# Performance work log

Hardware: AMD Instinct MI355X
Metric: run time of the kernel (lower is better)

## Reference

```python
import jax, jax.numpy as jnp
import numpy as np
from jax import lax

TEMPERATURE = 30.0
PAD = 1  # padding init-kwarg; stride=1, dilation=1


def setup_inputs() -> dict:
    key = jax.random.key(0)
    ks = jax.random.split(key, 8)
    B, D, HID, NF, K, CIN, COUT, HW = 32, 512, 256, 8, 3, 64, 64, 64
    return {
        "filter_condition_input": jax.random.normal(ks[0], (B, D), jnp.float32),
        "model_input": jax.random.normal(ks[1], (B, CIN, HW, HW), jnp.float32),
        "fc1_w": jax.random.normal(ks[2], (HID, D), jnp.float32) * (2.0 / D) ** 0.5,
        "fc1_b": jnp.zeros((HID,), jnp.float32),
        "fc2_w": jax.random.normal(ks[3], (NF, HID), jnp.float32) * (2.0 / HID) ** 0.5,
        "fc2_b": jnp.zeros((NF,), jnp.float32),
        "weight": jax.random.normal(ks[4], (NF, COUT, CIN, K, K), jnp.float32) * 0.05,
        "bias_p": jax.random.normal(ks[5], (NF, COUT), jnp.float32) * 0.05,
    }


def reference(filter_condition_input, model_input, fc1_w, fc1_b, fc2_w, fc2_b, weight, bias_p):
    # Routing MLP -> softmax attention over the num_filters kernel bank
    h = jax.nn.relu(filter_condition_input @ fc1_w.T + fc1_b)
    logits = h @ fc2_w.T + fc2_b
    attn = jax.nn.softmax(logits / TEMPERATURE, axis=1)  # [B, NF]

    # Per-sample aggregated conv kernels and biases
    agg_w = jnp.einsum("bf,foikl->boikl", attn, weight)  # [B, O, Cin, K, K]
    agg_b = attn @ bias_p                                  # [B, O]

    # groups = batch_size grouped conv == independent per-sample conv (vmapped)
    def conv1(x_i, w_i):  # x_i: [Cin,H,W], w_i: [O,Cin,K,K]
        return lax.conv_general_dilated(
            x_i[None], w_i, window_strides=(1, 1),
            padding=((PAD, PAD), (PAD, PAD)),
            dimension_numbers=("NCHW", "OIHW", "NCHW"))[0]

    out = jax.vmap(conv1)(model_input, agg_w) + agg_b[:, :, None, None]  # [B,O,H,W]
    return out, attn
```

## Files before the change

kernel.cpp:

```cpp
#include <hip/hip_runtime.h>
#include <hip/hip_bf16.h>

typedef __hip_bfloat16 bf16;
typedef unsigned short u16;
typedef unsigned int   u32;

#define B_    32
#define D_    512
#define HID_  256
#define NF_   8
#define CIN_  64
#define COUT_ 64
#define HW_   64
#define CONV_OUT_ELEMS (B_ * COUT_ * HW_ * HW_)
#define WBANK_ (NF_ * 36864)

typedef __attribute__((ext_vector_type(8))) short  short8;
typedef __attribute__((ext_vector_type(4))) float  floatx4;

__device__ inline float b2f(bf16 v) { return __bfloat162float(v); }
__device__ inline bf16  f2b(float f) { return __float2bfloat16(f); }
__device__ inline u16 f2bu(float f) { union { bf16 h; u16 u; } c; c.h = __float2bfloat16(f); return c.u; }
__device__ inline float bu2f(u16 u) { union { u32 i; float f; } c; c.i = ((u32)u) << 16; return c.f; }

__device__ inline float ldf(const void* p, int i, int isbf) {
    return isbf ? __bfloat162float(((const bf16*)p)[i]) : ((const float*)p)[i];
}

__device__ inline int word_bf16_sane(u32 v) {
    u32 lo = v & 0xFFFFu;
    u32 ex = (lo >> 7) & 0xFFu;
    return (lo == 0u || (ex >= 64u && ex <= 191u)) ? 1 : 0;
}

__global__ __launch_bounds__(256) void prep_kernel(
    const void* __restrict__ xin,
    const void* __restrict__ x,
    const void* __restrict__ fc1_w,
    const void* __restrict__ fc1_b,
    u16* __restrict__ xin_t,
    float* __restrict__ ws_hs)
{
    __shared__ u16 tr[64][66];
    __shared__ int fl[4];
    const int blk = blockIdx.x;
    const int t = threadIdx.x;

    if (blk < 2048) {
        const int b = blk >> 6, y = blk & 63;
        if (t == 0) fl[0] = 1;
        __syncthreads();
        if (t < 32) {
            u32 w = ((const u32*)xin)[t * 131072];
            if (!word_bf16_sane(w)) atomicAnd(&fl[0], 0);
        }
        __syncthreads();
        const int inbf = fl[0];

        const int ci = t >> 2, xq = (t & 3) * 16;
        u16 vals[16];
        if (inbf) {
            const bf16* src = (const bf16*)xin + (((b * CIN_ + ci) * HW_ + y) * HW_ + xq);
            uint4 v0 = *(const uint4*)src;
            uint4 v1 = *(const uint4*)(src + 8);
            const u32 w8[8] = { v0.x, v0.y, v0.z, v0.w, v1.x, v1.y, v1.z, v1.w };
#pragma unroll
            for (int k = 0; k < 8; ++k) {
                vals[2 * k]     = (u16)(w8[k] & 0xFFFF);
                vals[2 * k + 1] = (u16)(w8[k] >> 16);
            }
        } else {
            const float* src = (const float*)xin + (((b * CIN_ + ci) * HW_ + y) * HW_ + xq);
#pragma unroll
            for (int c = 0; c < 4; ++c) {
                float4 f = *(const float4*)(src + c * 4);
                vals[c * 4 + 0] = f2bu(f.x); vals[c * 4 + 1] = f2bu(f.y);
                vals[c * 4 + 2] = f2bu(f.z); vals[c * 4 + 3] = f2bu(f.w);
            }
        }
#pragma unroll
        for (int k = 0; k < 16; ++k) tr[xq + k][ci] = vals[k];
        __syncthreads();

        const int px = t >> 2, cg = (t & 3) * 16;
        u32 wd[8];
#pragma unroll
        for (int w = 0; w < 8; ++w)
            wd[w] = (u32)tr[px][cg + 2 * w] | ((u32)tr[px][cg + 2 * w + 1] << 16);
        u16* dst = xin_t + (((b * HW_ + y) * HW_ + px) * CIN_ + cg);
        ((uint4*)dst)[0] = make_uint4(wd[0], wd[1], wd[2], wd[3]);
        ((uint4*)dst)[1] = make_uint4(wd[4], wd[5], wd[6], wd[7]);
        return;
    }

    const int h = blk - 2048;
    const int b = t >> 3, seg = t & 7;
    if (t < 3) fl[t] = 1;
    __syncthreads();
    if (t < 96) {
        const int g = t >> 5, k = t & 31;
        const void* buf = (g == 0) ? x : (g == 1) ? fc1_w : fc1_b;
        const int elems = (g == 0) ? B_ * D_ : (g == 1) ? HID_ * D_ : HID_;
        const int nw = elems >> 1;
        const int n = nw < 32 ? nw : 32;
        if (k < n && nw >= 1) {
            u32 v = ((const u32*)buf)[k * (nw / n)];
            if (!word_bf16_sane(v)) atomicAnd(&fl[g], 0);
        }
    }
    __syncthreads();
    const int xbf = fl[0], wbf = fl[1], b1bf = fl[2];

    const int xoff = b * D_ + seg * 64;
    const int woff = h * D_ + seg * 64;
    float p = 0.f;
    if (!xbf && !wbf) {
        float4 xr[16], wr[16];
        const float4* xp = (const float4*)((const float*)x + xoff);
        const float4* wp = (const float4*)((const float*)fc1_w + woff);
#pragma unroll
        for (int c = 0; c < 16; ++c) xr[c] = xp[c];
#pragma unroll
        for (int c = 0; c < 16; ++c) wr[c] = wp[c];
#pragma unroll
        for (int c = 0; c < 16; ++c)
            p += xr[c].x * wr[c].x + xr[c].y * wr[c].y + xr[c].z * wr[c].z + xr[c].w * wr[c].w;
    } else if (xbf && wbf) {
        uint4 xr[8], wr[8];
        const uint4* xp = (const uint4*)((const bf16*)x + xoff);
        const uint4* wp = (const uint4*)((const bf16*)fc1_w + woff);
#pragma unroll
        for (int c = 0; c < 8; ++c) xr[c] = xp[c];
#pragma unroll
        for (int c = 0; c < 8; ++c) wr[c] = wp[c];
#pragma unroll
        for (int c = 0; c < 8; ++c) {
            const u32 xw[4] = { xr[c].x, xr[c].y, xr[c].z, xr[c].w };
            const u32 ww[4] = { wr[c].x, wr[c].y, wr[c].z, wr[c].w };
#pragma unroll
            for (int q2 = 0; q2 < 4; ++q2)
                p += bu2f((u16)(xw[q2] & 0xFFFF)) * bu2f((u16)(ww[q2] & 0xFFFF))
                   + bu2f((u16)(xw[q2] >> 16))    * bu2f((u16)(ww[q2] >> 16));
        }
    } else {
        for (int c = 0; c < 64; ++c) p += ldf(x, xoff + c, xbf) * ldf(fc1_w, woff + c, wbf);
    }
    p += __shfl_xor(p, 1);
    p += __shfl_xor(p, 2);
    p += __shfl_xor(p, 4);
    if (seg == 0) {
        p += ldf(fc1_b, h, b1bf);
        ws_hs[b * HID_ + h] = p > 0.f ? p : 0.f;
    }
}

__global__ __launch_bounds__(256) void agg2_kernel(
    const void* __restrict__ weight,
    const void* __restrict__ fc2_w,
    const void* __restrict__ fc2_b,
    const void* __restrict__ bias_p,
    const void* __restrict__ xin,
    const float* __restrict__ ws_hs,
    float* __restrict__ ws_aggb,
    u16* __restrict__ aggw,
    void* __restrict__ d_out)
{
    __shared__ float lds[2304];
    __shared__ float hs[HID_];
    __shared__ float at[NF_];
    __shared__ int   fl[5];
    const int t  = threadIdx.x;
    const int b  = blockIdx.x >> 4;
    const int o0 = (blockIdx.x & 15) * 4;

    if (t < 5) fl[t] = 1;
    hs[t] = ws_hs[b * HID_ + t];
    __syncthreads();
    if (t < 160) {
        const int g = t >> 5, k = t & 31;
        const void* buf = (g == 0) ? fc2_w : (g == 1) ? fc2_b : (g == 2) ? bias_p
                        : (g == 3) ? xin : weight;
        const int elems = (g == 0) ? NF_ * HID_ : (g == 1) ? NF_ : (g == 2) ? NF_ * COUT_
                        : (g == 3) ? B_ * CIN_ * HW_ * HW_ : WBANK_;
        const int nw = elems >> 1;
        const int n = nw < 32 ? nw : 32;
        if (k < n && nw >= 1) {
            u32 v = ((const u32*)buf)[k * (nw / n)];
            if (!word_bf16_sane(v)) atomicAnd(&fl[g], 0);
        }
    }
    __syncthreads();
    const int w2bf = fl[0], b2bf = fl[1], bpbf = fl[2], obf = fl[3], wbf = fl[4];

    {
        const int f = t >> 5, j = t & 31;
        const float* hp = hs + j * 8;
        float p;
        if (w2bf) {
            uint4 u = *(const uint4*)((const bf16*)fc2_w + f * HID_ + j * 8);
            p = bu2f((u16)(u.x & 0xFFFF)) * hp[0] + bu2f((u16)(u.x >> 16)) * hp[1]
              + bu2f((u16)(u.y & 0xFFFF)) * hp[2] + bu2f((u16)(u.y >> 16)) * hp[3]
              + bu2f((u16)(u.z & 0xFFFF)) * hp[4] + bu2f((u16)(u.z >> 16)) * hp[5]
              + bu2f((u16)(u.w & 0xFFFF)) * hp[6] + bu2f((u16)(u.w >> 16)) * hp[7];
        } else {
            const float* r = (const float*)fc2_w + f * HID_ + j * 8;
            float4 a = *(const float4*)r, c = *(const float4*)(r + 4);
            p = a.x * hp[0] + a.y * hp[1] + a.z * hp[2] + a.w * hp[3]
              + c.x * hp[4] + c.y * hp[5] + c.z * hp[6] + c.w * hp[7];
        }
#pragma unroll
        for (int m = 16; m; m >>= 1) p += __shfl_xor(p, m);
        if (j == 0) at[f] = (p + ldf(fc2_b, f, b2bf)) * (1.0f / 30.0f);
    }
    __syncthreads();
    if (t == 0) {
        float m = at[0];
#pragma unroll
        for (int ff = 1; ff < NF_; ++ff) m = fmaxf(m, at[ff]);
        float e[NF_], ssum = 0.f;
#pragma unroll
        for (int ff = 0; ff < NF_; ++ff) { e[ff] = __expf(at[ff] - m); ssum += e[ff]; }
        float inv = 1.0f / ssum;
#pragma unroll
        for (int ff = 0; ff < NF_; ++ff) at[ff] = e[ff] * inv;
    }
    __syncthreads();

    if ((blockIdx.x & 15) == 0 && t < NF_) {
        if (obf) ((bf16*)d_out)[CONV_OUT_ELEMS + b * NF_ + t] = f2b(at[t]);
        else    ((float*)d_out)[CONV_OUT_ELEMS + b * NF_ + t] = at[t];
    }
    if (t < 4) {
        const int o = o0 + t;
        float s = 0.f;
#pragma unroll
        for (int ff = 0; ff < NF_; ++ff) s += at[ff] * ldf(bias_p, ff * COUT_ + o, bpbf);
        ws_aggb[b * COUT_ + o] = s;
    }

#pragma unroll
    for (int j = 0; j < 9; ++j) {
        const int flat = t + 256 * j;
        const int o_l = flat / 576, rr = flat - o_l * 576;
        const int gbase = (o0 + o_l) * 576 + rr;
        float s = 0.f;
        if (wbf) {
#pragma unroll
            for (int f = 0; f < NF_; ++f) s += at[f] * b2f(((const bf16*)weight)[f * 36864 + gbase]);
        } else {
#pragma unroll
            for (int f = 0; f < NF_; ++f) s += at[f] * ((const float*)weight)[f * 36864 + gbase];
        }
        lds[flat] = s;
    }
    __syncthreads();
#pragma unroll
    for (int j = 0; j < 9; ++j) {
        const int e = t + 256 * j;
        const int tap = e >> 8, o_l = (e >> 6) & 3, ci = e & 63;
        aggw[b * 36864 + tap * 4096 + (o0 + o_l) * 64 + ci] = f2bu(lds[o_l * 576 + ci * 9 + tap]);
    }
}

__global__ __launch_bounds__(256) void conv_mfma4(
    const u16*  __restrict__ xin_t,
    const u16*  __restrict__ aggw,
    const float* __restrict__ aggb,
    const void* __restrict__ xin,
    void* __restrict__ out)
{
    __shared__ __align__(16) u16 smem[38880];
    __shared__ float bias_s[COUT_];
    __shared__ int s_ok;
    u16* A_s = smem;
    u16* B_s = smem + 23040;

    const int t    = threadIdx.x;
    const int bz   = blockIdx.x;
    const int b    = bz >> 4;
    const int y0   = (bz & 15) * 4;
    const int wv   = t >> 6;
    const int lane = t & 63, l15 = lane & 15, q = lane >> 4;

    if (t == 0) s_ok = 1;
    __syncthreads();
    if (t < 32) {
        u32 w = ((const u32*)xin)[t * 131072];
        if (!word_bf16_sane(w)) atomicAnd(&s_ok, 0);
    }
    if (t < COUT_) bias_s[t] = aggb[b * COUT_ + t];
    __syncthreads();
    const int outbf = s_ok;

    floatx4 acc[4][4];
#pragma unroll
    for (int mt = 0; mt < 4; ++mt)
#pragma unroll
        for (int nt = 0; nt < 4; ++nt) acc[mt][nt] = (floatx4)0.f;

    const u16* Abase = aggw + b * 36864;

    for (int ph = 0; ph < 2; ++ph) {
        const int ci0 = ph * 32;
#pragma unroll
        for (int j = 0; j < 9; ++j) {
            const int item = t + 256 * j;
            const int cg = item & 3, o = (item >> 2) & 63, tap = item >> 8;
            uint4 v = *(const uint4*)(Abase + tap * 4096 + o * 64 + ci0 + cg * 8);
            *(uint4*)&A_s[tap * 2560 + o * 40 + cg * 8] = v;
        }
#pragma unroll
        for (int j = 0; j < 7; ++j) {
            const int item = t + 256 * j;
            if (item < 1584) {
                const int cg = item & 3, col = (item >> 2) % 66, r = item / 264;
                const int gy = y0 - 1 + r, gx = col - 1;
                uint4 v = make_uint4(0, 0, 0, 0);
                if (gy >= 0 && gy < HW_ && gx >= 0 && gx < HW_)
                    v = *(const uint4*)(xin_t + (((b * HW_ + gy) * HW_ + gx) * CIN_ + ci0 + cg * 8));
                *(uint4*)&B_s[r * 2640 + col * 40 + cg * 8] = v;
            }
        }
        __syncthreads();
#pragma unroll
        for (int tap = 0; tap < 9; ++tap) {
            const int kh = tap / 3, kw = tap % 3;
            short8 af[4], bf[4];
#pragma unroll
            for (int mt = 0; mt < 4; ++mt)
                af[mt] = *(const short8*)&A_s[tap * 2560 + (mt * 16 + l15) * 40 + q * 8];
#pragma unroll
            for (int nt = 0; nt < 4; ++nt)
                bf[nt] = *(const short8*)&B_s[(wv + kh) * 2640 + (nt * 16 + l15 + kw) * 40 + q * 8];
#pragma unroll
            for (int mt = 0; mt < 4; ++mt)
#pragma unroll
                for (int nt = 0; nt < 4; ++nt)
                    acc[mt][nt] = __builtin_amdgcn_mfma_f32_16x16x32_bf16(
                        af[mt], bf[nt], acc[mt][nt], 0, 0, 0);
        }
        __syncthreads();
    }

    u16* out_s = smem;
#pragma unroll
    for (int mt = 0; mt < 4; ++mt) {
        floatx4 bb = *(const floatx4*)&bias_s[mt * 16 + q * 4];
#pragma unroll
        for (int nt = 0; nt < 4; ++nt) {
#pragma unroll
            for (int rg = 0; rg < 4; ++rg) {
                const float v = acc[mt][nt][rg] + bb[rg];
                out_s[(wv * 64 + (mt * 16 + q * 4 + rg)) * 68 + nt * 16 + l15] = f2bu(v);
            }
        }
    }
    __syncthreads();
#pragma unroll
    for (int j = 0; j < 16; ++j) {
        const int c = t + 256 * j;
        const int x0 = (c & 15) * 4, o = (c >> 4) & 63, w2 = c >> 10;
        const u16* src = &out_s[(w2 * 64 + o) * 68 + x0];
        const u16 h0 = src[0], h1 = src[1], h2 = src[2], h3 = src[3];
        const int gidx = ((b * COUT_ + o) * HW_ + (y0 + w2)) * HW_ + x0;
        if (outbf) {
            uint2 pk; pk.x = (u32)h0 | ((u32)h1 << 16); pk.y = (u32)h2 | ((u32)h3 << 16);
            *(uint2*)((u16*)out + gidx) = pk;
        } else {
            float4 f; f.x = bu2f(h0); f.y = bu2f(h1); f.z = bu2f(h2); f.w = bu2f(h3);
            *(float4*)((float*)out + gidx) = f;
        }
    }
}

extern "C" void kernel_launch(void* const* d_in, const int* in_sizes, int n_in,
                              void* d_out, int out_size, void* d_ws, size_t ws_size,
                              hipStream_t stream) {
    const void* x      = d_in[0];
    const void* xin    = d_in[1];
    const void* fc1_w  = d_in[2];
    const void* fc1_b  = d_in[3];
    const void* fc2_w  = d_in[4];
    const void* fc2_b  = d_in[5];
    const void* weight = d_in[6];
    const void* bias_p = d_in[7];

    float* ws      = (float*)d_ws;
    float* ws_aggb = ws + 256;
    float* ws_hs   = ws + 2304;
    u16*   ws_aggw = (u16*)(ws + 10496);
    u16*   ws_xint = (u16*)(ws + 600320);

    prep_kernel<<<dim3(2048 + HID_), dim3(256), 0, stream>>>(
        xin, x, fc1_w, fc1_b, ws_xint, ws_hs);

    agg2_kernel<<<dim3(B_ * 16), dim3(256), 0, stream>>>(
        weight, fc2_w, fc2_b, bias_p, xin, ws_hs, ws_aggb, ws_aggw, d_out);

    conv_mfma4<<<dim3(B_ * 16), dim3(256), 0, stream>>>(
        ws_xint, ws_aggw, ws_aggb, xin, d_out);
}
```

Baseline: 138.8 us.

## Fuse routing MLP and kernel aggregation into the input transpose kernel

Merges the prep and agg2 kernels into one launch. 32 extra blocks each compute one sample's full MLP, softmax, aggregated bias and aggregated weights, alongside the 2048 input-transpose blocks. This removes one kernel launch and the hidden-activation round trip through global memory. In exchange, each of those 32 blocks serially reads all of fc1_w and the whole 8x64x576 weight bank, where before that work was spread over 256 and 512 blocks. These long blocks could become the critical path of the fused kernel.

```diff
diff --git a/kernel.cpp b/kernel.cpp
--- a/kernel.cpp
+++ b/kernel.cpp
@@ -33,21 +33,30 @@
     return (lo == 0u || (ex >= 64u && ex <= 191u)) ? 1 : 0;
 }
 
-__global__ __launch_bounds__(256) void prep_kernel(
+__global__ __launch_bounds__(256) void prep_agg_kernel(
     const void* __restrict__ xin,
     const void* __restrict__ x,
     const void* __restrict__ fc1_w,
     const void* __restrict__ fc1_b,
+    const void* __restrict__ fc2_w,
+    const void* __restrict__ fc2_b,
+    const void* __restrict__ bias_p,
+    const void* __restrict__ weight,
     u16* __restrict__ xin_t,
-    float* __restrict__ ws_hs)
+    float* __restrict__ ws_aggb,
+    u16* __restrict__ aggw,
+    void* __restrict__ d_out)
 {
-    __shared__ u16 tr[64][66];
-    __shared__ int fl[4];
+    __shared__ __align__(16) u16 sm[18432];
+    __shared__ float xs[D_];
+    __shared__ float hs[HID_];
+    __shared__ float at[NF_];
+    __shared__ int   fl[8];
     const int blk = blockIdx.x;
     const int t = threadIdx.x;
 
-    if (blk < 2048) {
-        const int b = blk >> 6, y = blk & 63;
+    if (blk >= 32) {
+        const int bb = (blk - 32) >> 6, y = (blk - 32) & 63;
         if (t == 0) fl[0] = 1;
         __syncthreads();
         if (t < 32) {
@@ -56,11 +65,12 @@
         }
         __syncthreads();
         const int inbf = fl[0];
+        u16 (*tr)[66] = (u16(*)[66])sm;
 
         const int ci = t >> 2, xq = (t & 3) * 16;
         u16 vals[16];
         if (inbf) {
-            const bf16* src = (const bf16*)xin + (((b * CIN_ + ci) * HW_ + y) * HW_ + xq);
+            const bf16* src = (const bf16*)xin + (((bb * CIN_ + ci) * HW_ + y) * HW_ + xq);
             uint4 v0 = *(const uint4*)src;
             uint4 v1 = *(const uint4*)(src + 8);
             const u32 w8[8] = { v0.x, v0.y, v0.z, v0.w, v1.x, v1.y, v1.z, v1.w };
@@ -70,7 +80,7 @@
                 vals[2 * k + 1] = (u16)(w8[k] >> 16);
             }
         } else {
-            const float* src = (const float*)xin + (((b * CIN_ + ci) * HW_ + y) * HW_ + xq);
+            const float* src = (const float*)xin + (((bb * CIN_ + ci) * HW_ + y) * HW_ + xq);
 #pragma unroll
             for (int c = 0; c < 4; ++c) {
                 float4 f = *(const float4*)(src + c * 4);
@@ -87,110 +97,73 @@
 #pragma unroll
         for (int w = 0; w < 8; ++w)
             wd[w] = (u32)tr[px][cg + 2 * w] | ((u32)tr[px][cg + 2 * w + 1] << 16);
-        u16* dst = xin_t + (((b * HW_ + y) * HW_ + px) * CIN_ + cg);
+        u16* dst = xin_t + (((bb * HW_ + y) * HW_ + px) * CIN_ + cg);
         ((uint4*)dst)[0] = make_uint4(wd[0], wd[1], wd[2], wd[3]);
         ((uint4*)dst)[1] = make_uint4(wd[4], wd[5], wd[6], wd[7]);
         return;
     }
 
-    const int h = blk - 2048;
-    const int b = t >> 3, seg = t & 7;
-    if (t < 3) fl[t] = 1;
-    __syncthreads();
-    if (t < 96) {
+    const int b = blk;
+    if (t < 8) fl[t] = 1;
+    __syncthreads();
+    {
+        const void* bufs[8]  = { x, fc1_w, fc1_b, fc2_w, fc2_b, bias_p, weight, xin };
+        const int   elems[8] = { B_ * D_, HID_ * D_, HID_, NF_ * HID_, NF_,
+                                 NF_ * COUT_, WBANK_, B_ * CIN_ * HW_ * HW_ };
         const int g = t >> 5, k = t & 31;
-        const void* buf = (g == 0) ? x : (g == 1) ? fc1_w : fc1_b;
-        const int elems = (g == 0) ? B_ * D_ : (g == 1) ? HID_ * D_ : HID_;
-        const int nw = elems >> 1;
+        const int nw = elems[g] >> 1;
         const int n = nw < 32 ? nw : 32;
         if (k < n && nw >= 1) {
-            u32 v = ((const u32*)buf)[k * (nw / n)];
+            u32 v = ((const u32*)bufs[g])[k * (nw / n)];
             if (!word_bf16_sane(v)) atomicAnd(&fl[g], 0);
         }
     }
     __syncthreads();
-    const int xbf = fl[0], wbf = fl[1], b1bf = fl[2];
-
-    const int xoff = b * D_ + seg * 64;
-    const int woff = h * D_ + seg * 64;
-    float p = 0.f;
-    if (!xbf && !wbf) {
-        float4 xr[16], wr[16];
-        const float4* xp = (const float4*)((const float*)x + xoff);
-        const float4* wp = (const float4*)((const float*)fc1_w + woff);
-#pragma unroll
-        for (int c = 0; c < 16; ++c) xr[c] = xp[c];
-#pragma unroll
-        for (int c = 0; c < 16; ++c) wr[c] = wp[c];
-#pragma unroll
-        for (int c = 0; c < 16; ++c)
-            p += xr[c].x * wr[c].x + xr[c].y * wr[c].y + xr[c].z * wr[c].z + xr[c].w * wr[c].w;
-    } else if (xbf && wbf) {
-        uint4 xr[8], wr[8];
-        const uint4* xp = (const uint4*)((const bf16*)x + xoff);
-        const uint4* wp = (const uint4*)((const bf16*)fc1_w + woff);
-#pragma unroll
-        for (int c = 0; c < 8; ++c) xr[c] = xp[c];
-#pragma unroll
-        for (int c = 0; c < 8; ++c) wr[c] = wp[c];
-#pragma unroll
-        for (int c = 0; c < 8; ++c) {
-            const u32 xw[4] = { xr[c].x, xr[c].y, xr[c].z, xr[c].w };
-            const u32 ww[4] = { wr[c].x, wr[c].y, wr[c].z, wr[c].w };
-#pragma unroll
-            for (int q2 = 0; q2 < 4; ++q2)
-                p += bu2f((u16)(xw[q2] & 0xFFFF)) * bu2f((u16)(ww[q2] & 0xFFFF))
-                   + bu2f((u16)(xw[q2] >> 16))    * bu2f((u16)(ww[q2] >> 16));
-        }
-    } else {
-        for (int c = 0; c < 64; ++c) p += ldf(x, xoff + c, xbf) * ldf(fc1_w, woff + c, wbf);
-    }
-    p += __shfl_xor(p, 1);
-    p += __shfl_xor(p, 2);
-    p += __shfl_xor(p, 4);
-    if (seg == 0) {
-        p += ldf(fc1_b, h, b1bf);
-        ws_hs[b * HID_ + h] = p > 0.f ? p : 0.f;
-    }
-}
-
-__global__ __launch_bounds__(256) void agg2_kernel(
-    const void* __restrict__ weight,
-    const void* __restrict__ fc2_w,
-    const void* __restrict__ fc2_b,
-    const void* __restrict__ bias_p,
-    const void* __restrict__ xin,
-    const float* __restrict__ ws_hs,
-    float* __restrict__ ws_aggb,
-    u16* __restrict__ aggw,
-    void* __restrict__ d_out)
-{
-    __shared__ float lds[2304];
-    __shared__ float hs[HID_];
-    __shared__ float at[NF_];
-    __shared__ int   fl[5];
-    const int t  = threadIdx.x;
-    const int b  = blockIdx.x >> 4;
-    const int o0 = (blockIdx.x & 15) * 4;
-
-    if (t < 5) fl[t] = 1;
-    hs[t] = ws_hs[b * HID_ + t];
-    __syncthreads();
-    if (t < 160) {
-        const int g = t >> 5, k = t & 31;
-        const void* buf = (g == 0) ? fc2_w : (g == 1) ? fc2_b : (g == 2) ? bias_p
-                        : (g == 3) ? xin : weight;
-        const int elems = (g == 0) ? NF_ * HID_ : (g == 1) ? NF_ : (g == 2) ? NF_ * COUT_
-                        : (g == 3) ? B_ * CIN_ * HW_ * HW_ : WBANK_;
-        const int nw = elems >> 1;
-        const int n = nw < 32 ? nw : 32;
-        if (k < n && nw >= 1) {
-            u32 v = ((const u32*)buf)[k * (nw / n)];
-            if (!word_bf16_sane(v)) atomicAnd(&fl[g], 0);
-        }
-    }
-    __syncthreads();
-    const int w2bf = fl[0], b2bf = fl[1], bpbf = fl[2], obf = fl[3], wbf = fl[4];
+    const int xbf = fl[0], w1bf = fl[1], b1bf = fl[2], w2bf = fl[3];
+    const int b2bf = fl[4], bpbf = fl[5], wbf = fl[6], obf = fl[7];
+
+    for (int i = t; i < D_; i += 256) xs[i] = ldf(x, b * D_ + i, xbf);
+    __syncthreads();
+
+    const int seg = t & 7, hloc = t >> 3;
+    const float* xp = xs + seg * 64;
+#pragma unroll 2
+    for (int pass = 0; pass < 8; ++pass) {
+        const int h = pass * 32 + hloc;
+        const int woff = h * D_ + seg * 64;
+        float p = 0.f;
+        if (w1bf) {
+            uint4 wr[8];
+            const uint4* wp = (const uint4*)((const bf16*)fc1_w + woff);
+#pragma unroll
+            for (int c = 0; c < 8; ++c) wr[c] = wp[c];
+#pragma unroll
+            for (int c = 0; c < 8; ++c) {
+                const u32 ww[4] = { wr[c].x, wr[c].y, wr[c].z, wr[c].w };
+#pragma unroll
+                for (int q2 = 0; q2 < 4; ++q2)
+                    p += bu2f((u16)(ww[q2] & 0xFFFF)) * xp[c * 8 + q2 * 2]
+                       + bu2f((u16)(ww[q2] >> 16))    * xp[c * 8 + q2 * 2 + 1];
+            }
+        } else {
+            float4 wr[16];
+            const float4* wp = (const float4*)((const float*)fc1_w + woff);
+#pragma unroll
+            for (int c = 0; c < 16; ++c) wr[c] = wp[c];
+#pragma unroll
+            for (int c = 0; c < 16; ++c)
+                p += wr[c].x * xp[c * 4] + wr[c].y * xp[c * 4 + 1]
+                   + wr[c].z * xp[c * 4 + 2] + wr[c].w * xp[c * 4 + 3];
+        }
+        p += __shfl_xor(p, 1);
+        p += __shfl_xor(p, 2);
+        p += __shfl_xor(p, 4);
+        if (seg == 0) {
+            p += ldf(fc1_b, h, b1bf);
+            hs[h] = p > 0.f ? p : 0.f;
+        }
+    }
+    __syncthreads();
 
     {
         const int f = t >> 5, j = t & 31;
@@ -226,39 +199,44 @@
     }
     __syncthreads();
 
-    if ((blockIdx.x & 15) == 0 && t < NF_) {
+    if (t < NF_) {
         if (obf) ((bf16*)d_out)[CONV_OUT_ELEMS + b * NF_ + t] = f2b(at[t]);
         else    ((float*)d_out)[CONV_OUT_ELEMS + b * NF_ + t] = at[t];
     }
-    if (t < 4) {
-        const int o = o0 + t;
+    if (t < COUT_) {
         float s = 0.f;
 #pragma unroll
-        for (int ff = 0; ff < NF_; ++ff) s += at[ff] * ldf(bias_p, ff * COUT_ + o, bpbf);
-        ws_aggb[b * COUT_ + o] = s;
-    }
-
-#pragma unroll
-    for (int j = 0; j < 9; ++j) {
-        const int flat = t + 256 * j;
-        const int o_l = flat / 576, rr = flat - o_l * 576;
-        const int gbase = (o0 + o_l) * 576 + rr;
-        float s = 0.f;
-        if (wbf) {
-#pragma unroll
-            for (int f = 0; f < NF_; ++f) s += at[f] * b2f(((const bf16*)weight)[f * 36864 + gbase]);
-        } else {
-#pragma unroll
-            for (int f = 0; f < NF_; ++f) s += at[f] * ((const float*)weight)[f * 36864 + gbase];
-        }
-        lds[flat] = s;
-    }
-    __syncthreads();
-#pragma unroll
-    for (int j = 0; j < 9; ++j) {
-        const int e = t + 256 * j;
-        const int tap = e >> 8, o_l = (e >> 6) & 3, ci = e & 63;
-        aggw[b * 36864 + tap * 4096 + (o0 + o_l) * 64 + ci] = f2bu(lds[o_l * 576 + ci * 9 + tap]);
+        for (int ff = 0; ff < NF_; ++ff) s += at[ff] * ldf(bias_p, ff * COUT_ + t, bpbf);
+        ws_aggb[b * COUT_ + t] = s;
+    }
+
+    for (int p2 = 0; p2 < 2; ++p2) {
+        const int ci0 = p2 * 32;
+        __syncthreads();
+#pragma unroll 4
+        for (int j = 0; j < 72; ++j) {
+            const int i = t + 256 * j;
+            const int o = i / 288, rem = i - o * 288;
+            const int gbase = o * 576 + ci0 * 9 + rem;
+            float s = 0.f;
+            if (wbf) {
+#pragma unroll
+                for (int f = 0; f < NF_; ++f) s += at[f] * b2f(((const bf16*)weight)[f * 36864 + gbase]);
+            } else {
+#pragma unroll
+                for (int f = 0; f < NF_; ++f) s += at[f] * ((const float*)weight)[f * 36864 + gbase];
+            }
+            const int tap = rem % 9, ci_l = rem / 9;
+            sm[tap * 2048 + o * 32 + ci_l] = f2bu(s);
+        }
+        __syncthreads();
+#pragma unroll
+        for (int j = 0; j < 9; ++j) {
+            const int e = t + 256 * j;
+            const int cg = e & 3, o = (e >> 2) & 63, tap = e >> 8;
+            uint4 v = *(const uint4*)&sm[tap * 2048 + o * 32 + cg * 8];
+            *(uint4*)(aggw + b * 36864 + tap * 4096 + o * 64 + ci0 + cg * 8) = v;
+        }
     }
 }
 
@@ -387,15 +365,12 @@
 
     float* ws      = (float*)d_ws;
     float* ws_aggb = ws + 256;
-    float* ws_hs   = ws + 2304;
     u16*   ws_aggw = (u16*)(ws + 10496);
     u16*   ws_xint = (u16*)(ws + 600320);
 
-    prep_kernel<<<dim3(2048 + HID_), dim3(256), 0, stream>>>(
-        xin, x, fc1_w, fc1_b, ws_xint, ws_hs);
-
-    agg2_kernel<<<dim3(B_ * 16), dim3(256), 0, stream>>>(
-        weight, fc2_w, fc2_b, bias_p, xin, ws_hs, ws_aggb, ws_aggw, d_out);
+    prep_agg_kernel<<<dim3(32 + 2048), dim3(256), 0, stream>>>(
+        xin, x, fc1_w, fc1_b, fc2_w, fc2_b, bias_p, weight,
+        ws_xint, ws_aggb, ws_aggw, d_out);
 
     conv_mfma4<<<dim3(B_ * 16), dim3(256), 0, stream>>>(
         ws_xint, ws_aggw, ws_aggb, xin, d_out);
```

After: 194.8 us. +40.4%, slower.
